# Kernel tuning notes

Hardware: AMD Instinct MI355X
Metric: run time of the kernel (lower is better)

Reference implementation:

```python
import jax, jax.numpy as jnp
import numpy as np

N_NODES = 50000
N_PAIRS = 400000
F_IN = 5
GCN_DIMS = [32, 64, 128]
MLP_DIMS = [128, 64]


def _lin_init(key, out_d, in_d):
    return jax.random.normal(key, (out_d, in_d), dtype=jnp.float32) / np.sqrt(in_d)


def setup_inputs() -> dict:
    rng = np.random.default_rng(0)
    hi = rng.integers(1, N_NODES, size=N_PAIRS)
    lo = rng.integers(0, 2**31 - 1, size=N_PAIRS) % hi  # lo < hi strictly
    # each undirected pair appears twice per direction (two parallel edges / classes)
    src = np.concatenate([hi, hi, lo, lo]).astype(np.int32)
    dst = np.concatenate([lo, lo, hi, hi]).astype(np.int32)
    edges = jnp.asarray(np.stack([src, dst]))  # [2, 4P]
    detector_labels = jnp.asarray(rng.random(N_NODES) < 0.9)
    key = jax.random.key(0)
    ks = jax.random.split(key, 16)
    x = jax.random.normal(ks[0], (N_NODES, F_IN), dtype=jnp.float32)
    edge_attr = jax.random.uniform(ks[1], (4 * N_PAIRS, 2), dtype=jnp.float32)
    inp = {"x": x, "edges": edges, "edge_attr": edge_attr, "detector_labels": detector_labels}
    dims = [F_IN] + GCN_DIMS
    for i, (di, do) in enumerate(zip(dims[:-1], dims[1:])):
        inp[f"gc{i}_Wrel"] = _lin_init(ks[2 + 3 * i], do, di)
        inp[f"gc{i}_brel"] = jnp.zeros((do,), dtype=jnp.float32)
        inp[f"gc{i}_Wroot"] = _lin_init(ks[3 + 3 * i], do, di)
    mdims = [2 * GCN_DIMS[-1] + 1] + MLP_DIMS
    for i, (di, do) in enumerate(zip(mdims[:-1], mdims[1:])):
        inp[f"fc{i}_W"] = _lin_init(ks[11 + 2 * i], do, di)
        inp[f"fc{i}_b"] = jnp.zeros((do,), dtype=jnp.float32)
    inp["out_W"] = _lin_init(ks[15], 1, MLP_DIMS[-1])
    inp["out_b"] = jnp.zeros((1,), dtype=jnp.float32)
    return inp


def _edge_perm(edges_np, det_np):
    # SplitSyndromes: keep edges with both endpoints in detector set, src > dst,
    # then sort_edge_index (stable lexicographic sort by (src, dst)).
    src, dst = edges_np[0], edges_np[1]
    valid = det_np[src] & det_np[dst] & (src > dst)
    idx = np.where(valid)[0]
    order = np.lexsort((dst[idx], src[idx]))
    return idx[order]


def reference(x, edges, edge_attr, detector_labels,
              gc0_Wrel, gc0_brel, gc0_Wroot,
              gc1_Wrel, gc1_brel, gc1_Wroot,
              gc2_Wrel, gc2_brel, gc2_Wroot,
              fc0_W, fc0_b, fc1_W, fc1_b, out_W, out_b):
    src, dst = edges[0], edges[1]
    w = edge_attr[:, 0] * edge_attr[:, 1]  # GraphConv edge weight
    # GraphConv: lin_rel(sum_j w_ji * x_j) + lin_root(x), ReLU
    for Wrel, brel, Wroot in ((gc0_Wrel, gc0_brel, gc0_Wroot),
                              (gc1_Wrel, gc1_brel, gc1_Wroot),
                              (gc2_Wrel, gc2_brel, gc2_Wroot)):
        agg = jax.ops.segment_sum(x[src] * w[:, None], dst, num_segments=N_NODES)
        x = jax.nn.relu(agg @ Wrel.T + brel + x @ Wroot.T)
    perm = _edge_perm(np.asarray(edges), np.asarray(detector_labels))
    e_src = edges[0, perm]
    e_dst = edges[1, perm]
    ea = edge_attr[perm]  # [M, 2]
    feat = jnp.concatenate([x[e_src], ea[:, :1], x[e_dst]], axis=-1)  # [M, 257]
    for W, b in ((fc0_W, fc0_b), (fc1_W, fc1_b)):
        feat = jax.nn.relu(feat @ W.T + b)
    score = feat @ out_W.T + out_b  # [M, 1]
    pair = jnp.concatenate([score[::2], score[1::2]], axis=1)  # [M/2, 2]
    cls = jnp.stack([ea[::2, 1], ea[1::2, 1]], axis=1)  # [M/2, 2]
    mi = jnp.argmin(pair, axis=1)
    sel = jnp.take_along_axis(pair, mi[:, None], axis=1)[:, 0]
    cls_sel = jnp.take_along_axis(cls, mi[:, None], axis=1)[:, 0]
    edges_out = jnp.stack([e_src[::2], e_dst[::2]])
    return edges_out, jax.nn.sigmoid(sel), cls_sel
```

## Files before the change

kernel.cpp:

```cpp
#include <hip/hip_runtime.h>
#include <hip/hip_bf16.h>
#include <stdint.h>

typedef unsigned long long ull;
typedef unsigned short us;
typedef __attribute__((ext_vector_type(8))) short short8;
typedef __attribute__((ext_vector_type(4))) float f32x4;
#define IDX_BITS 22
#define IDX_MASK 0x3FFFFFu

__device__ __forceinline__ float bfq(float x) {
    return __bfloat162float(__float2bfloat16(x));
}
__device__ __forceinline__ us bfu(float x) {
    __hip_bfloat16 b = __float2bfloat16(x);
    return *(us*)&b;
}
__device__ __forceinline__ float b2f(us u) {
    return __bfloat162float(*(__hip_bfloat16*)&u);
}
__device__ __forceinline__ float ldx(const float* p, size_t i) { return p[i]; }
__device__ __forceinline__ float ldx(const us* p, size_t i) { return b2f(p[i]); }


__global__ void k_det8(const int* __restrict__ src, const int* __restrict__ dst,
                       const unsigned char* __restrict__ det, int P, int* __restrict__ stats,
                       int* __restrict__ dcnt) {
    __shared__ int blkc;
    if (threadIdx.x == 0) blkc = 0;
    __syncthreads();
    int e = blockIdx.x * blockDim.x + threadIdx.x;
    bool v = false;
    if (e < P) {
        int hi = src[e], lo = dst[e];
        atomicAdd(&dcnt[lo], 1);
        atomicAdd(&dcnt[hi], 1);
        v = (det[hi] != 0) && (det[lo] != 0);
    }
    ull b = __ballot(v);
    if ((threadIdx.x & 63) == 0 && b) atomicAdd(&blkc, (int)__popcll(b));
    __syncthreads();
    if (threadIdx.x == 0 && blkc) atomicAdd(&stats[0], blkc);
}
__global__ void k_det16(const int* __restrict__ src, const int* __restrict__ dst,
                        const us* __restrict__ det, int P, int* __restrict__ stats) {
    if (stats[3] != -1) return;
    __shared__ int blkc;
    if (threadIdx.x == 0) blkc = 0;
    __syncthreads();
    int e = blockIdx.x * blockDim.x + threadIdx.x;
    bool v = false;
    if (e < P) v = (det[src[e]] != 0) && (det[dst[e]] != 0);
    ull b = __ballot(v);
    if ((threadIdx.x & 63) == 0 && b) atomicAdd(&blkc, (int)__popcll(b));
    __syncthreads();
    if (threadIdx.x == 0 && blkc) atomicAdd(&stats[1], blkc);
}
__global__ void k_det32(const int* __restrict__ src, const int* __restrict__ dst,
                        const unsigned int* __restrict__ det, int P, int* __restrict__ stats) {
    if (stats[3] != -2) return;
    __shared__ int blkc;
    if (threadIdx.x == 0) blkc = 0;
    __syncthreads();
    int e = blockIdx.x * blockDim.x + threadIdx.x;
    bool v = false;
    if (e < P) v = (det[src[e]] != 0) && (det[dst[e]] != 0);
    ull b = __ballot(v);
    if ((threadIdx.x & 63) == 0 && b) atomicAdd(&blkc, (int)__popcll(b));
    __syncthreads();
    if (threadIdx.x == 0 && blkc) atomicAdd(&stats[2], blkc);
}
__global__ void k_mode(int* stats, int osz, int step) {
    if (step == 1) {
        int c = stats[0];
        stats[3] = (c == osz / 4 || c == osz / 2) ? 0 : -1;
    } else if (step == 2) {
        if (stats[3] == -1) {
            int c = stats[1];
            stats[3] = (c == osz / 4 || c == osz / 2) ? 2 : -2;
        }
    } else {
        if (stats[3] == -2) stats[3] = 1;
        int m = stats[3];
        stats[4] = (m == 0) ? stats[0] : (m == 2) ? stats[1] : stats[2];
    }
}
__device__ __forceinline__ bool det_ok(int n, const void* det, int mode) {
    if (mode == 0) return ((const unsigned char*)det)[n] != 0;
    if (mode == 2) return ((const us*)det)[n] != 0;
    return ((const unsigned int*)det)[n] != 0;
}

__global__ __launch_bounds__(1024) void k_scanA(const int* __restrict__ cnt,
                                                int* __restrict__ off,
                                                int* __restrict__ bsum, int n) {
    __shared__ int wsum[16];
    int t = threadIdx.x, lane = t & 63, w = t >> 6;
    int i = blockIdx.x * 1024 + t;
    int v = (i < n) ? cnt[i] : 0;
    int inc = v;
#pragma unroll
    for (int s = 1; s < 64; s <<= 1) {
        int u = __shfl_up(inc, s);
        if (lane >= s) inc += u;
    }
    if (lane == 63) wsum[w] = inc;
    __syncthreads();
    if (t < 16) {
        int x = wsum[t], sc = x;
#pragma unroll
        for (int s = 1; s < 16; s <<= 1) {
            int u = __shfl_up(sc, s);
            if (t >= s) sc += u;
        }
        wsum[t] = sc - x;
    }
    __syncthreads();
    if (i < n) off[i] = wsum[w] + inc - v;
    if (t == 1023) bsum[blockIdx.x] = wsum[15] + inc;
}
__global__ void k_scanB(int* __restrict__ bsum, int* __restrict__ off, int nb, int n) {
    int t = threadIdx.x;
    int v = (t < nb) ? bsum[t] : 0;
    int inc = v;
#pragma unroll
    for (int s = 1; s < 64; s <<= 1) {
        int u = __shfl_up(inc, s);
        if (t >= s) inc += u;
    }
    if (t < nb) bsum[t] = inc - v;
    if (t == 63) off[n] = inc;
}
__global__ __launch_bounds__(1024) void k_scanC(int* __restrict__ off,
                                                const int* __restrict__ bsum, int n) {
    int i = blockIdx.x * 1024 + threadIdx.x;
    if (i < n && blockIdx.x > 0) off[i] += bsum[blockIdx.x];
}

__global__ void k_scatter(const int* __restrict__ src, const int* __restrict__ dst,
                          const float* __restrict__ ea, const int* __restrict__ off,
                          int* __restrict__ cur, int2* __restrict__ epair,
                          const void* __restrict__ det, const int* __restrict__ stats,
                          int* __restrict__ scnt, int P) {
    int e = blockIdx.x * blockDim.x + threadIdx.x;
    if (e >= P) return;
    int hi = src[e], lo = dst[e];
    float w1 = ea[2 * e] * ea[2 * e + 1] + ea[2 * (e + P)] * ea[2 * (e + P) + 1];
    float w2 = ea[2 * (2 * P + e)] * ea[2 * (2 * P + e) + 1] +
               ea[2 * (3 * P + e)] * ea[2 * (3 * P + e) + 1];
    int p1 = off[lo] + atomicAdd(&cur[lo], 1);
    epair[p1] = make_int2(hi, __float_as_int(w1));
    int p2 = off[hi] + atomicAdd(&cur[hi], 1);
    epair[p2] = make_int2(lo, __float_as_int(w2));
    int mode = stats[3];
    if (det_ok(hi, det, mode) && det_ok(lo, det, mode)) atomicAdd(&scnt[hi], 1);
}

__global__ void k_packall(const float* __restrict__ W1rel, const float* __restrict__ W1root,
                          const float* __restrict__ W2rel, const float* __restrict__ W2root,
                          const float* __restrict__ W3rel, const float* __restrict__ W3root,
                          const float* __restrict__ W0, const float* __restrict__ Wfc1,
                          us* __restrict__ pb1, us* __restrict__ pb2, us* __restrict__ pb3,
                          us* __restrict__ pbP, us* __restrict__ pbQ, us* __restrict__ w1f) {
    int gid = blockIdx.x * blockDim.x + threadIdx.x;
    const float* Wrel;
    const float* Wroot;
    us* out;
    int idx, FIN, CT;
    if (gid < 1024) { idx = gid; Wrel = W1rel; Wroot = W1root; out = pb1; FIN = 5; CT = 2; }
    else if (gid < 5120) { idx = gid - 1024; Wrel = W2rel; Wroot = W2root; out = pb2; FIN = 32; CT = 4; }
    else if (gid < 21504) { idx = gid - 5120; Wrel = W3rel; Wroot = W3root; out = pb3; FIN = 64; CT = 8; }
    else if (gid < 54272) {
        int i2 = gid - 21504;
        bool isQ = i2 >= 16384;
        int i = i2 & 16383;
        int j = i & 7, l = (i >> 3) & 63, ct = (i >> 9) & 7, ks = i >> 12;
        int k = ks * 32 + ((l >> 4) << 3) + j;
        int col = ct * 16 + (l & 15);
        float v = isQ ? W0[col * 257 + 129 + k] : W0[col * 257 + k];
        (isQ ? pbQ : pbP)[i] = bfu(v);
        return;
    } else if (gid < 62464) {
        int i = gid - 54272;
        int j = i & 7, l = (i >> 3) & 63, ct = (i >> 9) & 3, ks = i >> 11;
        int k = ks * 32 + ((l >> 4) << 3) + j;
        int col = ct * 16 + (l & 15);
        w1f[i] = bfu(Wfc1[col * 128 + k]);
        return;
    } else return;
    int j = idx & 7, l = (idx >> 3) & 63;
    int t = idx >> 9;
    int ct = t % CT, ks = t / CT;
    int k = ks * 32 + ((l >> 4) << 3) + j;
    int col = ct * 16 + (l & 15);
    float v = 0.f;
    if (k < FIN) v = Wrel[col * FIN + k];
    else if (k < 2 * FIN) v = Wroot[col * FIN + (k - FIN)];
    out[idx] = bfu(v);
}

template <int FIN, int KP, int G, typename TIN>
__global__ __launch_bounds__(256) void k_agg(
    const TIN* __restrict__ xin, const int2* __restrict__ epair,
    const int* __restrict__ doff, us* __restrict__ A, int N) {
    int tid = blockIdx.x * 256 + threadIdx.x;
    int n = tid / G, f = tid % G;
    if (n >= N) return;
    us* row = &A[(size_t)n * KP];
    if (f < FIN) {
        int b = doff[n], e2 = doff[n + 1];
        float a = 0.f;
        int j = b;
        for (; j + 8 <= e2; j += 8) {
            int2 pp[8];
#pragma unroll
            for (int u = 0; u < 8; ++u) pp[u] = epair[j + u];
            float xv[8];
#pragma unroll
            for (int u = 0; u < 8; ++u) xv[u] = ldx(xin, (size_t)pp[u].x * FIN + f);
#pragma unroll
            for (int u = 0; u < 8; ++u) a = fmaf(__int_as_float(pp[u].y), xv[u], a);
        }
        for (; j < e2; ++j) {
            int2 pq = epair[j];
            a = fmaf(__int_as_float(pq.y), ldx(xin, (size_t)pq.x * FIN + f), a);
        }
        row[f] = bfu(a);
        row[FIN + f] = bfu(ldx(xin, (size_t)n * FIN + f));
    }
    for (int c = 2 * FIN + f; c < KP; c += G) row[c] = 0;
}

template <int KP, int FOUT>
__global__ __launch_bounds__(256) void k_mm(
    const us* __restrict__ A, const us* __restrict__ bfrag,
    const float* __restrict__ bias, us* __restrict__ xout, int N) {
    constexpr int CT = FOUT / 16, KS = KP / 32, STR = KP + 8, CPR = KP / 8;
    __shared__ us Al[64 * STR];
    int t = threadIdx.x, lane = t & 63, w = t >> 6;
    int n0 = blockIdx.x * 64;
    for (int idx = t; idx < 64 * CPR; idx += 256) {
        int r = idx / CPR, c = idx % CPR;
        int n = n0 + r;
        uint4 v = (n < N) ? *(const uint4*)&A[(size_t)n * KP + c * 8] : make_uint4(0, 0, 0, 0);
        *(uint4*)&Al[r * STR + c * 8] = v;
    }
    __syncthreads();
    f32x4 acc[CT];
#pragma unroll
    for (int ct = 0; ct < CT; ++ct) acc[ct] = (f32x4){0.f, 0.f, 0.f, 0.f};
    int arow = w * 16 + (lane & 15);
    int koff = (lane >> 4) << 3;
#pragma unroll
    for (int ks = 0; ks < KS; ++ks) {
        short8 a = *(const short8*)&Al[arow * STR + ks * 32 + koff];
#pragma unroll
        for (int ct = 0; ct < CT; ++ct) {
            short8 b = ((const short8*)bfrag)[(ks * CT + ct) * 64 + lane];
            acc[ct] = __builtin_amdgcn_mfma_f32_16x16x32_bf16(a, b, acc[ct], 0, 0, 0);
        }
    }
    int g = lane >> 4, c0 = lane & 15;
#pragma unroll
    for (int ct = 0; ct < CT; ++ct) {
        int col = ct * 16 + c0;
        float bb = bias[col];
#pragma unroll
        for (int r2 = 0; r2 < 4; ++r2) {
            int n = n0 + w * 16 + g * 4 + r2;
            if (n < N) xout[(size_t)n * FOUT + col] = bfu(fmaxf(acc[ct][r2] + bb, 0.f));
        }
    }
}

__global__ __launch_bounds__(256) void k_mmPQ(
    const us* __restrict__ x3b, const us* __restrict__ pbP, const us* __restrict__ pbQ,
    const float* __restrict__ b0, us* __restrict__ P, us* __restrict__ Q, int N) {
    constexpr int CT = 8, KS = 4, STR = 136, CPR = 16;
    __shared__ us Al[64 * STR];
    int t = threadIdx.x, lane = t & 63, w = t >> 6;
    int n0 = blockIdx.x * 64;
    for (int idx = t; idx < 64 * CPR; idx += 256) {
        int r = idx / CPR, c = idx % CPR;
        int n = n0 + r;
        uint4 v = (n < N) ? *(const uint4*)&x3b[(size_t)n * 128 + c * 8] : make_uint4(0, 0, 0, 0);
        *(uint4*)&Al[r * STR + c * 8] = v;
    }
    __syncthreads();
    int arow = w * 16 + (lane & 15);
    int koff = (lane >> 4) << 3;
    int g = lane >> 4, c0 = lane & 15;
    f32x4 acc[CT];
#pragma unroll
    for (int ct = 0; ct < CT; ++ct) acc[ct] = (f32x4){0.f, 0.f, 0.f, 0.f};
#pragma unroll
    for (int ks = 0; ks < KS; ++ks) {
        short8 a = *(const short8*)&Al[arow * STR + ks * 32 + koff];
#pragma unroll
        for (int ct = 0; ct < CT; ++ct) {
            short8 b = ((const short8*)pbP)[(ks * CT + ct) * 64 + lane];
            acc[ct] = __builtin_amdgcn_mfma_f32_16x16x32_bf16(a, b, acc[ct], 0, 0, 0);
        }
    }
#pragma unroll
    for (int ct = 0; ct < CT; ++ct) {
        int col = ct * 16 + c0;
        float bb = b0[col];
#pragma unroll
        for (int r2 = 0; r2 < 4; ++r2) {
            int n = n0 + w * 16 + g * 4 + r2;
            if (n < N) P[(size_t)n * 128 + col] = bfu(acc[ct][r2] + bb);
        }
    }
#pragma unroll
    for (int ct = 0; ct < CT; ++ct) acc[ct] = (f32x4){0.f, 0.f, 0.f, 0.f};
#pragma unroll
    for (int ks = 0; ks < KS; ++ks) {
        short8 a = *(const short8*)&Al[arow * STR + ks * 32 + koff];
#pragma unroll
        for (int ct = 0; ct < CT; ++ct) {
            short8 b = ((const short8*)pbQ)[(ks * CT + ct) * 64 + lane];
            acc[ct] = __builtin_amdgcn_mfma_f32_16x16x32_bf16(a, b, acc[ct], 0, 0, 0);
        }
    }
#pragma unroll
    for (int ct = 0; ct < CT; ++ct) {
        int col = ct * 16 + c0;
#pragma unroll
        for (int r2 = 0; r2 < 4; ++r2) {
            int n = n0 + w * 16 + g * 4 + r2;
            if (n < N) Q[(size_t)n * 128 + col] = bfu(acc[ct][r2]);
        }
    }
}

__global__ void k_scatter_ent(const int* __restrict__ src, const int* __restrict__ dst,
                              const void* __restrict__ det, const int* __restrict__ stats,
                              const int* __restrict__ off, int* __restrict__ cur,
                              ull* __restrict__ ent, int P, int Mcap) {
    int e = blockIdx.x * blockDim.x + threadIdx.x;
    if (e >= P) return;
    int hi = src[e], lo = dst[e];
    int mode = stats[3];
    if (det_ok(hi, det, mode) && det_ok(lo, det, mode)) {
        int p = off[hi] + atomicAdd(&cur[hi], 1);
        if (p < Mcap) ent[p] = ((ull)(unsigned)lo << IDX_BITS) | (unsigned)e;
    }
}

__global__ __launch_bounds__(256) void k_wsort(const int* __restrict__ off,
                                               ull* __restrict__ ent, int N, int Mcap) {
    int node = blockIdx.x * 4 + (threadIdx.x >> 6);
    int lane = threadIdx.x & 63;
    if (node >= N) return;
    int b = off[node], e2 = off[node + 1];
    if (e2 > Mcap) e2 = Mcap;
    int len = e2 - b;
    if (len <= 1) return;
    if (len <= 64) {
        ull key = (lane < len) ? ent[b + lane] : ~0ull;
        int phases = len + (len & 1);
        for (int ph = 0; ph < phases; ++ph) {
            int partner;
            if ((ph & 1) == 0) partner = lane ^ 1;
            else partner = (lane == 0 || lane == 63) ? lane
                                                     : ((lane & 1) ? lane + 1 : lane - 1);
            ull other = __shfl(key, partner);
            if (partner > lane) key = key < other ? key : other;
            else if (partner < lane) key = key > other ? key : other;
        }
        if (lane < len) ent[b + lane] = key;
    } else if (lane == 0) {
        for (int i = b + 1; i < e2; ++i) {
            ull k = ent[i];
            int j = i - 1;
            while (j >= b && ent[j] > k) { ent[j + 1] = ent[j]; --j; }
            ent[j + 1] = k;
        }
    }
}

__global__ __launch_bounds__(256) void k_mlp2(
    const us* __restrict__ Pm, const us* __restrict__ Qm, const float* __restrict__ ea,
    const int* __restrict__ src, const ull* __restrict__ ent, const int* __restrict__ stats,
    const float* __restrict__ W0, const us* __restrict__ w1f,
    const float* __restrict__ b1, const float* __restrict__ w2, const float* __restrict__ b2,
    float* __restrict__ scores, int P) {
    int Mh = stats[4];
    int rows = 2 * Mh;
    int m0 = blockIdx.x * 64;
    if (m0 >= rows) return;
    __shared__ us A[64 * 136];
    __shared__ float ws0e[128];
    int t = threadIdx.x, lane = t & 63, w = t >> 6;
    if (t < 128) ws0e[t] = W0[t * 257 + 128];
    __syncthreads();

    {
        int j = t >> 3, q = t & 7;
        int pr = (m0 >> 1) + j;
        if (pr < Mh) {
            ull en = ent[pr];
            int e = (int)(en & IDX_MASK);
            int lo = (int)(en >> IDX_BITS);
            int hi = src[e];
            float eaA = ea[2 * e];
            float eaB = ea[2 * (e + P)];
            const us* Pr = Pm + (size_t)hi * 128 + q * 16;
            const us* Qr = Qm + (size_t)lo * 128 + q * 16;
#pragma unroll
            for (int h = 0; h < 2; ++h) {
                int cb = q * 16 + h * 8;
                short8 pv = *(const short8*)&Pr[h * 8];
                short8 qv = *(const short8*)&Qr[h * 8];
                short8 ra, rb;
#pragma unroll
                for (int i = 0; i < 8; ++i) {
                    float base = b2f((us)pv[i]) + b2f((us)qv[i]);
                    float we = ws0e[cb + i];
                    ra[i] = (short)bfu(fmaxf(base + eaA * we, 0.f));
                    rb[i] = (short)bfu(fmaxf(base + eaB * we, 0.f));
                }
                *(short8*)&A[(2 * j) * 136 + cb] = ra;
                *(short8*)&A[(2 * j + 1) * 136 + cb] = rb;
            }
        } else {
            uint4 z = make_uint4(0, 0, 0, 0);
            *(uint4*)&A[(2 * j) * 136 + q * 16] = z;
            *(uint4*)&A[(2 * j) * 136 + q * 16 + 8] = z;
            *(uint4*)&A[(2 * j + 1) * 136 + q * 16] = z;
            *(uint4*)&A[(2 * j + 1) * 136 + q * 16 + 8] = z;
        }
    }
    __syncthreads();

    f32x4 acc1[4];
#pragma unroll
    for (int ct = 0; ct < 4; ++ct) acc1[ct] = (f32x4){0.f, 0.f, 0.f, 0.f};
    {
        int arow = w * 16 + (lane & 15);
        int koff = (lane >> 4) << 3;
#pragma unroll
        for (int ks = 0; ks < 4; ++ks) {
            short8 a = *(const short8*)&A[arow * 136 + ks * 32 + koff];
#pragma unroll
            for (int ct = 0; ct < 4; ++ct) {
                short8 b = ((const short8*)w1f)[(ks * 4 + ct) * 64 + lane];
                acc1[ct] = __builtin_amdgcn_mfma_f32_16x16x32_bf16(a, b, acc1[ct], 0, 0, 0);
            }
        }
    }
    {
        int g = lane >> 4, c0 = lane & 15;
        float part[4] = {0.f, 0.f, 0.f, 0.f};
#pragma unroll
        for (int ct = 0; ct < 4; ++ct) {
            int col = ct * 16 + c0;
            float bb = b1[col], wv = w2[col];
#pragma unroll
            for (int r = 0; r < 4; ++r)
                part[r] += fmaxf(acc1[ct][r] + bb, 0.f) * wv;
        }
        float bout = b2[0];
#pragma unroll
        for (int r = 0; r < 4; ++r) {
            float v = part[r];
            v += __shfl_xor(v, 1);
            v += __shfl_xor(v, 2);
            v += __shfl_xor(v, 4);
            v += __shfl_xor(v, 8);
            if (c0 == 0) {
                int m = m0 + w * 16 + g * 4 + r;
                if (m < rows) scores[m] = v + bout;
            }
        }
    }
}

__global__ void k_pair(const ull* __restrict__ ent, const float* __restrict__ scores,
                       const int* __restrict__ src, const float* __restrict__ ea,
                       const int* __restrict__ stats, float* __restrict__ out, int P) {
    int Mh = stats[4];
    int p = blockIdx.x * blockDim.x + threadIdx.x;
    if (p >= Mh) return;
    ull en = ent[p];
    int e0 = (int)(en & IDX_MASK);
    int lo = (int)(en >> IDX_BITS);
    int hi = src[e0];
    float s0 = scores[2 * p], s1 = scores[2 * p + 1];
    int pick = (s1 < s0) ? 1 : 0;
    float sel = pick ? s1 : s0;
    int ep = pick ? (e0 + P) : e0;
    float cls = ea[2 * ep + 1];
    float sig = 1.f / (1.f + expf(-sel));
    out[p] = bfq((float)hi);
    out[Mh + p] = bfq((float)lo);
    out[2 * Mh + p] = bfq(sig);
    out[3 * Mh + p] = bfq(cls);
}

extern "C" void kernel_launch(void* const* d_in, const int* in_sizes, int n_in,
                              void* d_out, int out_size, void* d_ws, size_t ws_size,
                              hipStream_t stream) {
    const float* x0 = (const float*)d_in[0];
    const int* edges = (const int*)d_in[1];
    const float* ea = (const float*)d_in[2];
    const void* det = d_in[3];

    int N = in_sizes[0] / 5;
    int E = in_sizes[1] / 2;
    int P = E / 4;
    int osz = out_size;
    int Mcap = osz;

    const int* src = edges;
    const int* dst = edges + E;

    char* p = (char*)d_ws;
    auto alloc = [&](size_t bytes) {
        char* r = p;
        p += (bytes + 255) & ~(size_t)255;
        return r;
    };
    us* xa = (us*)alloc((size_t)N * 32 * 2);
    us* xb = (us*)alloc((size_t)N * 64 * 2);
    us* x3b = (us*)alloc((size_t)N * 128 * 2);
    us* Abuf = (us*)alloc((size_t)N * 128 * 2);
    us* Pb = Abuf;
    us* Qb = (us*)alloc((size_t)N * 128 * 2);
    us* pb1 = (us*)alloc(1024 * 2);
    us* pb2 = (us*)alloc(4096 * 2);
    us* pb3 = (us*)alloc(16384 * 2);
    us* pbP = (us*)alloc(16384 * 2);
    us* pbQ = (us*)alloc(16384 * 2);
    us* w1f = (us*)alloc(8192 * 2);
    int* bsum = (int*)alloc(256);
    char* z0 = p;
    int* stats = (int*)alloc(256);
    int* dcnt = (int*)alloc((size_t)N * 4);
    int* dcur = (int*)alloc((size_t)N * 4);
    int* scnt = (int*)alloc((size_t)N * 4);
    int* scur = (int*)alloc((size_t)N * 4);
    size_t zlen = (size_t)(p - z0);
    char* u0 = p;
    int* doff = (int*)alloc((size_t)(N + 1) * 4);
    int2* epair = (int2*)alloc((size_t)(2 * P) * 8);
    char* endB = p;
    p = u0;
    int* soff = (int*)alloc((size_t)(N + 1) * 4);
    ull* ent = (ull*)alloc((size_t)Mcap * 8);
    float* scores = (float*)alloc((size_t)Mcap * 4);
    char* endC = p;
    size_t need = (size_t)(((endB > endC) ? endB : endC) - (char*)d_ws);
    if (need > ws_size) return;

    const int B = 256;
    int gP = (P + B - 1) / B;
    int nb = (N + 1023) / 1024;

    hipMemsetAsync(z0, 0, zlen, stream);

    k_det8<<<gP, B, 0, stream>>>(src, dst, (const unsigned char*)det, P, stats, dcnt);
    k_mode<<<1, 1, 0, stream>>>(stats, osz, 1);
    k_det16<<<gP, B, 0, stream>>>(src, dst, (const us*)det, P, stats);
    k_mode<<<1, 1, 0, stream>>>(stats, osz, 2);
    k_det32<<<gP, B, 0, stream>>>(src, dst, (const unsigned int*)det, P, stats);
    k_mode<<<1, 1, 0, stream>>>(stats, osz, 3);

    k_packall<<<(62464 + B - 1) / B, B, 0, stream>>>(
        (const float*)d_in[4], (const float*)d_in[6],
        (const float*)d_in[7], (const float*)d_in[9],
        (const float*)d_in[10], (const float*)d_in[12],
        (const float*)d_in[13], (const float*)d_in[15],
        pb1, pb2, pb3, pbP, pbQ, w1f);

    k_scanA<<<nb, 1024, 0, stream>>>(dcnt, doff, bsum, N);
    k_scanB<<<1, 64, 0, stream>>>(bsum, doff, nb, N);
    k_scanC<<<nb, 1024, 0, stream>>>(doff, bsum, N);

    k_scatter<<<gP, B, 0, stream>>>(src, dst, ea, doff, dcur, epair, det, stats, scnt, P);

    k_agg<5, 32, 8, float><<<((size_t)N * 8 + B - 1) / B, B, 0, stream>>>(
        x0, epair, doff, Abuf, N);
    k_mm<32, 32><<<(N + 63) / 64, B, 0, stream>>>(Abuf, pb1, (const float*)d_in[5], xa, N);
    k_agg<32, 64, 32, us><<<((size_t)N * 32 + B - 1) / B, B, 0, stream>>>(
        xa, epair, doff, Abuf, N);
    k_mm<64, 64><<<(N + 63) / 64, B, 0, stream>>>(Abuf, pb2, (const float*)d_in[8], xb, N);
    k_agg<64, 128, 64, us><<<((size_t)N * 64 + B - 1) / B, B, 0, stream>>>(
        xb, epair, doff, Abuf, N);
    k_mm<128, 128><<<(N + 63) / 64, B, 0, stream>>>(Abuf, pb3, (const float*)d_in[11], x3b, N);

    k_mmPQ<<<(N + 63) / 64, B, 0, stream>>>(x3b, pbP, pbQ, (const float*)d_in[14], Pb, Qb, N);

    k_scanA<<<nb, 1024, 0, stream>>>(scnt, soff, bsum, N);
    k_scanB<<<1, 64, 0, stream>>>(bsum, soff, nb, N);
    k_scanC<<<nb, 1024, 0, stream>>>(soff, bsum, N);
    k_scatter_ent<<<gP, B, 0, stream>>>(src, dst, det, stats, soff, scur, ent, P, Mcap);
    k_wsort<<<(N + 3) / 4, B, 0, stream>>>(soff, ent, N, Mcap);

    k_mlp2<<<(osz + 63) / 64, B, 0, stream>>>(
        Pb, Qb, ea, src, ent, stats,
        (const float*)d_in[13], w1f,
        (const float*)d_in[16], (const float*)d_in[17], (const float*)d_in[18],
        scores, P);

    k_pair<<<(osz / 2 + B - 1) / B, B, 0, stream>>>(ent, scores, src, ea, stats,
                                                    (float*)d_out, P);
}
```

Baseline: 386.8 us.

## Record atomic ranks during counting and fuse pair selection into the MLP kernel

The counting kernel now stores the slot index returned by each atomicAdd, for both the degree histogram and the valid-edge histogram. The later scatter kernels compute positions from the offsets plus these saved ranks, so they no longer need their own atomics or the second cursor arrays. Pair selection (argmin, sigmoid, class pick and output writes) moves into the MLP epilogue, which removes the scores buffer and the separate pair kernel. The cost is extra rank arrays held in memory, plus fix-up kernels that recompute the valid histogram when the detector dtype is not bytes.

Measured after the change: 333.0 us. -13.9%, faster.

```diff
diff --git a/kernel.cpp b/kernel.cpp
--- a/kernel.cpp
+++ b/kernel.cpp
@@ -25,7 +25,8 @@
 
 __global__ void k_det8(const int* __restrict__ src, const int* __restrict__ dst,
                        const unsigned char* __restrict__ det, int P, int* __restrict__ stats,
-                       int* __restrict__ dcnt) {
+                       int* __restrict__ dcnt, int* __restrict__ scnt,
+                       int2* __restrict__ rnk, int* __restrict__ vrnk) {
     __shared__ int blkc;
     if (threadIdx.x == 0) blkc = 0;
     __syncthreads();
@@ -33,9 +34,11 @@
     bool v = false;
     if (e < P) {
         int hi = src[e], lo = dst[e];
-        atomicAdd(&dcnt[lo], 1);
-        atomicAdd(&dcnt[hi], 1);
+        int r1 = atomicAdd(&dcnt[lo], 1);
+        int r2 = atomicAdd(&dcnt[hi], 1);
+        rnk[e] = make_int2(r1, r2);
         v = (det[hi] != 0) && (det[lo] != 0);
+        vrnk[e] = v ? atomicAdd(&scnt[hi], 1) : -1;
     }
     ull b = __ballot(v);
     if ((threadIdx.x & 63) == 0 && b) atomicAdd(&blkc, (int)__popcll(b));
@@ -91,6 +94,23 @@
     return ((const unsigned int*)det)[n] != 0;
 }
 
+__global__ void k_fixzero(const int* __restrict__ stats, int* __restrict__ scnt, int N) {
+    if (stats[3] == 0) return;
+    int i = blockIdx.x * blockDim.x + threadIdx.x;
+    if (i < N) scnt[i] = 0;
+}
+__global__ void k_fixhist(const int* __restrict__ src, const int* __restrict__ dst,
+                          const void* __restrict__ det, const int* __restrict__ stats,
+                          int* __restrict__ scnt, int* __restrict__ vrnk, int P) {
+    int m = stats[3];
+    if (m == 0) return;
+    int e = blockIdx.x * blockDim.x + threadIdx.x;
+    if (e >= P) return;
+    int hi = src[e], lo = dst[e];
+    bool v = det_ok(hi, det, m) && det_ok(lo, det, m);
+    vrnk[e] = v ? atomicAdd(&scnt[hi], 1) : -1;
+}
+
 __global__ __launch_bounds__(1024) void k_scanA(const int* __restrict__ cnt,
                                                 int* __restrict__ off,
                                                 int* __restrict__ bsum, int n) {
@@ -138,22 +158,17 @@
 }
 
 __global__ void k_scatter(const int* __restrict__ src, const int* __restrict__ dst,
-                          const float* __restrict__ ea, const int* __restrict__ off,
-                          int* __restrict__ cur, int2* __restrict__ epair,
-                          const void* __restrict__ det, const int* __restrict__ stats,
-                          int* __restrict__ scnt, int P) {
+                          const float* __restrict__ ea, const int* __restrict__ doff,
+                          const int2* __restrict__ rnk, int2* __restrict__ epair, int P) {
     int e = blockIdx.x * blockDim.x + threadIdx.x;
     if (e >= P) return;
     int hi = src[e], lo = dst[e];
     float w1 = ea[2 * e] * ea[2 * e + 1] + ea[2 * (e + P)] * ea[2 * (e + P) + 1];
     float w2 = ea[2 * (2 * P + e)] * ea[2 * (2 * P + e) + 1] +
                ea[2 * (3 * P + e)] * ea[2 * (3 * P + e) + 1];
-    int p1 = off[lo] + atomicAdd(&cur[lo], 1);
-    epair[p1] = make_int2(hi, __float_as_int(w1));
-    int p2 = off[hi] + atomicAdd(&cur[hi], 1);
-    epair[p2] = make_int2(lo, __float_as_int(w2));
-    int mode = stats[3];
-    if (det_ok(hi, det, mode) && det_ok(lo, det, mode)) atomicAdd(&scnt[hi], 1);
+    int2 r = rnk[e];
+    epair[doff[lo] + r.x] = make_int2(hi, __float_as_int(w1));
+    epair[doff[hi] + r.y] = make_int2(lo, __float_as_int(w2));
 }
 
 __global__ void k_packall(const float* __restrict__ W1rel, const float* __restrict__ W1root,
@@ -335,17 +350,15 @@
 }
 
 __global__ void k_scatter_ent(const int* __restrict__ src, const int* __restrict__ dst,
-                              const void* __restrict__ det, const int* __restrict__ stats,
-                              const int* __restrict__ off, int* __restrict__ cur,
+                              const int* __restrict__ vrnk, const int* __restrict__ soff,
                               ull* __restrict__ ent, int P, int Mcap) {
     int e = blockIdx.x * blockDim.x + threadIdx.x;
     if (e >= P) return;
+    int rv = vrnk[e];
+    if (rv < 0) return;
     int hi = src[e], lo = dst[e];
-    int mode = stats[3];
-    if (det_ok(hi, det, mode) && det_ok(lo, det, mode)) {
-        int p = off[hi] + atomicAdd(&cur[hi], 1);
-        if (p < Mcap) ent[p] = ((ull)(unsigned)lo << IDX_BITS) | (unsigned)e;
-    }
+    int p = soff[hi] + rv;
+    if (p < Mcap) ent[p] = ((ull)(unsigned)lo << IDX_BITS) | (unsigned)e;
 }
 
 __global__ __launch_bounds__(256) void k_wsort(const int* __restrict__ off,
@@ -385,13 +398,15 @@
     const int* __restrict__ src, const ull* __restrict__ ent, const int* __restrict__ stats,
     const float* __restrict__ W0, const us* __restrict__ w1f,
     const float* __restrict__ b1, const float* __restrict__ w2, const float* __restrict__ b2,
-    float* __restrict__ scores, int P) {
+    float* __restrict__ out, int P) {
     int Mh = stats[4];
     int rows = 2 * Mh;
     int m0 = blockIdx.x * 64;
     if (m0 >= rows) return;
     __shared__ us A[64 * 136];
     __shared__ float ws0e[128];
+    __shared__ int pHi[32], pLo[32];
+    __shared__ float clsA[32], clsB[32];
     int t = threadIdx.x, lane = t & 63, w = t >> 6;
     if (t < 128) ws0e[t] = W0[t * 257 + 128];
     __syncthreads();
@@ -406,6 +421,12 @@
             int hi = src[e];
             float eaA = ea[2 * e];
             float eaB = ea[2 * (e + P)];
+            if (q == 0) {
+                pHi[j] = hi;
+                pLo[j] = lo;
+                clsA[j] = ea[2 * e + 1];
+                clsB[j] = ea[2 * (e + P) + 1];
+            }
             const us* Pr = Pm + (size_t)hi * 128 + q * 16;
             const us* Qr = Qm + (size_t)lo * 128 + q * 16;
 #pragma unroll
@@ -462,6 +483,7 @@
                 part[r] += fmaxf(acc1[ct][r] + bb, 0.f) * wv;
         }
         float bout = b2[0];
+        float sv[4];
 #pragma unroll
         for (int r = 0; r < 4; ++r) {
             float v = part[r];
@@ -469,34 +491,27 @@
             v += __shfl_xor(v, 2);
             v += __shfl_xor(v, 4);
             v += __shfl_xor(v, 8);
-            if (c0 == 0) {
-                int m = m0 + w * 16 + g * 4 + r;
-                if (m < rows) scores[m] = v + bout;
+            sv[r] = v + bout;
+        }
+        if (c0 == 0) {
+#pragma unroll
+            for (int rr = 0; rr < 4; rr += 2) {
+                int jloc = (w * 16 + g * 4 + rr) >> 1;
+                int pgi = (m0 >> 1) + jloc;
+                if (pgi < Mh) {
+                    float s0 = sv[rr], s1 = sv[rr + 1];
+                    int pick = (s1 < s0) ? 1 : 0;
+                    float sel = pick ? s1 : s0;
+                    float cls = pick ? clsB[jloc] : clsA[jloc];
+                    float sig = 1.f / (1.f + expf(-sel));
+                    out[pgi] = bfq((float)pHi[jloc]);
+                    out[Mh + pgi] = bfq((float)pLo[jloc]);
+                    out[2 * Mh + pgi] = bfq(sig);
+                    out[3 * Mh + pgi] = bfq(cls);
+                }
             }
         }
     }
-}
-
-__global__ void k_pair(const ull* __restrict__ ent, const float* __restrict__ scores,
-                       const int* __restrict__ src, const float* __restrict__ ea,
-                       const int* __restrict__ stats, float* __restrict__ out, int P) {
-    int Mh = stats[4];
-    int p = blockIdx.x * blockDim.x + threadIdx.x;
-    if (p >= Mh) return;
-    ull en = ent[p];
-    int e0 = (int)(en & IDX_MASK);
-    int lo = (int)(en >> IDX_BITS);
-    int hi = src[e0];
-    float s0 = scores[2 * p], s1 = scores[2 * p + 1];
-    int pick = (s1 < s0) ? 1 : 0;
-    float sel = pick ? s1 : s0;
-    int ep = pick ? (e0 + P) : e0;
-    float cls = ea[2 * ep + 1];
-    float sig = 1.f / (1.f + expf(-sel));
-    out[p] = bfq((float)hi);
-    out[Mh + p] = bfq((float)lo);
-    out[2 * Mh + p] = bfq(sig);
-    out[3 * Mh + p] = bfq(cls);
 }
 
 extern "C" void kernel_launch(void* const* d_in, const int* in_sizes, int n_in,
@@ -535,12 +550,12 @@
     us* pbQ = (us*)alloc(16384 * 2);
     us* w1f = (us*)alloc(8192 * 2);
     int* bsum = (int*)alloc(256);
+    int2* rnk = (int2*)alloc((size_t)P * 8);
+    int* vrnk = (int*)alloc((size_t)P * 4);
     char* z0 = p;
     int* stats = (int*)alloc(256);
     int* dcnt = (int*)alloc((size_t)N * 4);
-    int* dcur = (int*)alloc((size_t)N * 4);
     int* scnt = (int*)alloc((size_t)N * 4);
-    int* scur = (int*)alloc((size_t)N * 4);
     size_t zlen = (size_t)(p - z0);
     char* u0 = p;
     int* doff = (int*)alloc((size_t)(N + 1) * 4);
@@ -549,7 +564,6 @@
     p = u0;
     int* soff = (int*)alloc((size_t)(N + 1) * 4);
     ull* ent = (ull*)alloc((size_t)Mcap * 8);
-    float* scores = (float*)alloc((size_t)Mcap * 4);
     char* endC = p;
     size_t need = (size_t)(((endB > endC) ? endB : endC) - (char*)d_ws);
     if (need > ws_size) return;
@@ -560,12 +574,15 @@
 
     hipMemsetAsync(z0, 0, zlen, stream);
 
-    k_det8<<<gP, B, 0, stream>>>(src, dst, (const unsigned char*)det, P, stats, dcnt);
+    k_det8<<<gP, B, 0, stream>>>(src, dst, (const unsigned char*)det, P, stats,
+                                 dcnt, scnt, rnk, vrnk);
     k_mode<<<1, 1, 0, stream>>>(stats, osz, 1);
     k_det16<<<gP, B, 0, stream>>>(src, dst, (const us*)det, P, stats);
     k_mode<<<1, 1, 0, stream>>>(stats, osz, 2);
     k_det32<<<gP, B, 0, stream>>>(src, dst, (const unsigned int*)det, P, stats);
     k_mode<<<1, 1, 0, stream>>>(stats, osz, 3);
+    k_fixzero<<<(N + B - 1) / B, B, 0, stream>>>(stats, scnt, N);
+    k_fixhist<<<gP, B, 0, stream>>>(src, dst, det, stats, scnt, vrnk, P);
 
     k_packall<<<(62464 + B - 1) / B, B, 0, stream>>>(
         (const float*)d_in[4], (const float*)d_in[6],
@@ -578,7 +595,7 @@
     k_scanB<<<1, 64, 0, stream>>>(bsum, doff, nb, N);
     k_scanC<<<nb, 1024, 0, stream>>>(doff, bsum, N);
 
-    k_scatter<<<gP, B, 0, stream>>>(src, dst, ea, doff, dcur, epair, det, stats, scnt, P);
+    k_scatter<<<gP, B, 0, stream>>>(src, dst, ea, doff, rnk, epair, P);
 
     k_agg<5, 32, 8, float><<<((size_t)N * 8 + B - 1) / B, B, 0, stream>>>(
         x0, epair, doff, Abuf, N);
@@ -595,15 +612,12 @@
     k_scanA<<<nb, 1024, 0, stream>>>(scnt, soff, bsum, N);
     k_scanB<<<1, 64, 0, stream>>>(bsum, soff, nb, N);
     k_scanC<<<nb, 1024, 0, stream>>>(soff, bsum, N);
-    k_scatter_ent<<<gP, B, 0, stream>>>(src, dst, det, stats, soff, scur, ent, P, Mcap);
+    k_scatter_ent<<<gP, B, 0, stream>>>(src, dst, vrnk, soff, ent, P, Mcap);
     k_wsort<<<(N + 3) / 4, B, 0, stream>>>(soff, ent, N, Mcap);
 
     k_mlp2<<<(osz + 63) / 64, B, 0, stream>>>(
         Pb, Qb, ea, src, ent, stats,
         (const float*)d_in[13], w1f,
         (const float*)d_in[16], (const float*)d_in[17], (const float*)d_in[18],
-        scores, P);
-
-    k_pair<<<(osz / 2 + B - 1) / B, B, 0, stream>>>(ent, scores, src, ea, stats,
-                                                    (float*)d_out, P);
-}
+        (float*)d_out, P);
+}
```
